# Optimization experiments

Hardware: AMD Instinct MI355X
Metric: run time of the kernel (lower is better)

Reference implementation:

```python
import jax, jax.numpy as jnp
import numpy as np

B, S, D = 2, 2048, 1024
H = 16
HD = D // H  # head_dim = 64


def setup_inputs() -> dict:
    key = jax.random.key(0)
    ks = jax.random.split(key, 9)
    std = 1.0 / np.sqrt(HD)
    inp = {
        "X": jax.random.normal(ks[0], (B, S, D), dtype=jnp.float32),
        # per-head Q/K/V Linear weights stacked: [H, head_dim, head_dim], biases [H, head_dim]
        "Wq": jax.random.uniform(ks[1], (H, HD, HD), jnp.float32, -std, std),
        "bq": jax.random.uniform(ks[2], (H, HD), jnp.float32, -std, std),
        "Wk": jax.random.uniform(ks[3], (H, HD, HD), jnp.float32, -std, std),
        "bk": jax.random.uniform(ks[4], (H, HD), jnp.float32, -std, std),
        "Wv": jax.random.uniform(ks[5], (H, HD, HD), jnp.float32, -std, std),
        "bv": jax.random.uniform(ks[6], (H, HD), jnp.float32, -std, std),
        # output projection: [D, D] (in, out layout), bias [D]
        "Wo": jax.random.uniform(ks[7], (D, D), jnp.float32, -1.0 / np.sqrt(D), 1.0 / np.sqrt(D)),
        "bo": jax.random.uniform(ks[8], (D,), jnp.float32, -1.0 / np.sqrt(D), 1.0 / np.sqrt(D)),
    }
    return inp


def reference(X, Wq, bq, Wk, bk, Wv, bv, Wo, bo):
    # Split hidden dim into heads: [B, S, H, HD]
    x = X.reshape(B, S, H, HD)
    scale = jnp.sqrt(jnp.asarray(HD, dtype=X.dtype))
    # Per-head linear projections (batched over heads)
    Q = jnp.einsum("bshd,hde->bshe", x, Wq) + bq
    K = jnp.einsum("bshd,hde->bshe", x, Wk) + bk
    V = jnp.einsum("bshd,hde->bshe", x, Wv) + bv
    # Attention scores [B, H, S, S]
    scores = jnp.einsum("bshd,bthd->bhst", Q, K) / scale
    attn = jax.nn.softmax(scores, axis=-1)
    # Weighted values -> [B, S, H, HD] -> concat -> [B, S, D]
    out = jnp.einsum("bhst,bthd->bshd", attn, V).reshape(B, S, D)
    return out @ Wo + bo
```

## Files before the change

kernel.cpp:

```cpp
#include <hip/hip_runtime.h>
#include <stdint.h>

#define B_  2
#define S_  2048
#define D_  1024
#define H_  16
#define HD_ 64
#define TOK (B_*S_)

typedef __bf16 bf16x8 __attribute__((ext_vector_type(8)));
typedef __bf16 bf16x4 __attribute__((ext_vector_type(4)));
typedef float  f32x4  __attribute__((ext_vector_type(4)));

static_assert(sizeof(bf16x8) == 16, "bf16x8 must be 16B");
static_assert(sizeof(bf16x4) == 8,  "bf16x4 must be 8B");

__device__ __forceinline__ float fexp2(float x) { return __builtin_amdgcn_exp2f(x); }

__device__ __forceinline__ f32x4 mfma16(bf16x8 a, bf16x8 b, f32x4 c) {
    return __builtin_amdgcn_mfma_f32_16x16x32_bf16(a, b, c, 0, 0, 0);
}

__global__ __launch_bounds__(256) void k_transpose_wo(
    const float* __restrict__ Wo, unsigned short* __restrict__ WoT)
{
    __shared__ float t[64][65];
    const int i0 = blockIdx.x * 64;
    const int o0 = blockIdx.y * 64;
    const int tid = threadIdx.x;
    #pragma unroll
    for (int p = 0; p < 16; ++p) {
        int idx = tid + p * 256;
        int r = idx >> 6, c = idx & 63;
        t[r][c] = Wo[(size_t)(i0 + r) * D_ + o0 + c];
    }
    __syncthreads();
    #pragma unroll
    for (int p = 0; p < 16; ++p) {
        int idx = tid + p * 256;
        int r = idx >> 6, c = idx & 63;
        reinterpret_cast<__bf16*>(WoT)[(size_t)(o0 + r) * D_ + i0 + c] = (__bf16)t[c][r];
    }
}

__global__ __launch_bounds__(256) void k_transpose_w(
    const float* __restrict__ Wq, const float* __restrict__ Wk,
    const float* __restrict__ Wv, unsigned short* __restrict__ WT)
{
    __shared__ float t[64][65];
    const int h = blockIdx.x, z = blockIdx.y;
    const float* W = (z == 0) ? Wq : (z == 1) ? Wk : Wv;
    const int tid = threadIdx.x;
    #pragma unroll
    for (int p = 0; p < 4; ++p) {
        int idx = tid + p * 256;
        int r = idx >> 4, c4 = (idx & 15) * 4;
        *reinterpret_cast<float4*>(&t[r][c4]) =
            *reinterpret_cast<const float4*>(&W[h * 4096 + r * 64 + c4]);
    }
    __syncthreads();
    const int e = tid >> 2, db = (tid & 3) * 16;
    __bf16* out = reinterpret_cast<__bf16*>(WT) + ((size_t)(z * H_ + h) * 64 + e) * 64 + db;
    #pragma unroll
    for (int jj = 0; jj < 2; ++jj) {
        bf16x8 v;
        #pragma unroll
        for (int j = 0; j < 8; ++j) v[j] = (__bf16)t[db + jj * 8 + j][e];
        *reinterpret_cast<bf16x8*>(out + jj * 8) = v;
    }
}

__global__ __launch_bounds__(256) void k_qkv(
    const float* __restrict__ X, const unsigned short* __restrict__ WT,
    const float* __restrict__ bq, const float* __restrict__ bk,
    const float* __restrict__ bv,
    unsigned short* __restrict__ Qo, unsigned short* __restrict__ Ko,
    unsigned short* __restrict__ Vt)
{
    __shared__ unsigned short Xl[128 * 64];
    __shared__ unsigned short Wl[3][64 * 64];

    const int tid  = threadIdx.x;
    const int lane = tid & 63, w = tid >> 6;
    const int g = lane >> 4, q = lane & 15;
    const int tok0 = blockIdx.x * 128;
    const int h    = blockIdx.y;

    #pragma unroll
    for (int i = 0; i < 4; ++i) {
        int c = tid + 256 * i;
        int row = c >> 3, slot = c & 7;
        const float* src = &X[(size_t)(tok0 + row) * D_ + h * HD_ + slot * 8];
        float4 x0 = *reinterpret_cast<const float4*>(src);
        float4 x1 = *reinterpret_cast<const float4*>(src + 4);
        bf16x8 v = { (__bf16)x0.x, (__bf16)x0.y, (__bf16)x0.z, (__bf16)x0.w,
                     (__bf16)x1.x, (__bf16)x1.y, (__bf16)x1.z, (__bf16)x1.w };
        *reinterpret_cast<bf16x8*>(
            reinterpret_cast<char*>(Xl) + row * 128 + ((slot ^ (row & 7)) * 16)) = v;
    }
    #pragma unroll
    for (int zz = 0; zz < 3; ++zz) {
        #pragma unroll
        for (int i = 0; i < 2; ++i) {
            int c = tid + 256 * i;
            int e = c >> 3, slot = c & 7;
            bf16x8 v = *reinterpret_cast<const bf16x8*>(
                &WT[((size_t)(zz * H_ + h) * 64 + e) * 64 + slot * 8]);
            *reinterpret_cast<bf16x8*>(
                reinterpret_cast<char*>(Wl[zz]) + e * 128 + ((slot ^ (e & 7)) * 16)) = v;
        }
    }
    __syncthreads();

    const float scq = 0.18033688011112042f;
    const int b  = tok0 >> 11;
    const int sb = (tok0 & (S_ - 1)) + w * 32;

    #pragma unroll
    for (int z = 0; z < 3; ++z) {
        const float* bb = (z == 0) ? bq : (z == 1) ? bk : bv;
        f32x4 acc[2][4] = {};
        #pragma unroll
        for (int s = 0; s < 2; ++s) {
            bf16x8 af[2], bfr[4];
            #pragma unroll
            for (int am = 0; am < 2; ++am) {
                int row  = w * 32 + am * 16 + q;
                int slot = (s * 4 + g) ^ (row & 7);
                af[am] = *reinterpret_cast<const bf16x8*>(
                    reinterpret_cast<const char*>(Xl) + row * 128 + slot * 16);
            }
            #pragma unroll
            for (int bn = 0; bn < 4; ++bn) {
                int row  = bn * 16 + q;
                int slot = (s * 4 + g) ^ (row & 7);
                bfr[bn] = *reinterpret_cast<const bf16x8*>(
                    reinterpret_cast<const char*>(Wl[z]) + row * 128 + slot * 16);
            }
            if (z == 2) {
                #pragma unroll
                for (int am = 0; am < 2; ++am)
                    #pragma unroll
                    for (int bn = 0; bn < 4; ++bn)
                        acc[am][bn] = mfma16(af[am], bfr[bn], acc[am][bn]);
            } else {
                #pragma unroll
                for (int am = 0; am < 2; ++am)
                    #pragma unroll
                    for (int bn = 0; bn < 4; ++bn)
                        acc[am][bn] = mfma16(bfr[bn], af[am], acc[am][bn]);
            }
        }
        if (z == 2) {
            #pragma unroll
            for (int bn = 0; bn < 4; ++bn) {
                int e = bn * 16 + q;
                float bia = bb[h * HD_ + e];
                #pragma unroll
                for (int am = 0; am < 2; ++am) {
                    int s4 = sb + am * 16 + 4 * g;
                    bf16x4 ov = { (__bf16)(acc[am][bn][0] + bia), (__bf16)(acc[am][bn][1] + bia),
                                  (__bf16)(acc[am][bn][2] + bia), (__bf16)(acc[am][bn][3] + bia) };
                    *reinterpret_cast<bf16x4*>(
                        &Vt[((size_t)(b * H_ + h) * HD_ + e) * S_ + s4]) = ov;
                }
            }
        } else {
            const float sc = (z == 0) ? scq : 1.0f;
            unsigned short* dst = (z == 0) ? Qo : Ko;
            #pragma unroll
            for (int bn = 0; bn < 4; ++bn) {
                float4 bia4 = *reinterpret_cast<const float4*>(&bb[h * HD_ + bn * 16 + 4 * g]);
                #pragma unroll
                for (int am = 0; am < 2; ++am) {
                    int tok = sb + am * 16 + q;
                    bf16x4 ov = { (__bf16)((acc[am][bn][0] + bia4.x) * sc),
                                  (__bf16)((acc[am][bn][1] + bia4.y) * sc),
                                  (__bf16)((acc[am][bn][2] + bia4.z) * sc),
                                  (__bf16)((acc[am][bn][3] + bia4.w) * sc) };
                    *reinterpret_cast<bf16x4*>(
                        &dst[((size_t)(b * H_ + h) * S_ + tok) * HD_ + bn * 16 + 4 * g]) = ov;
                }
            }
        }
    }
}

__global__ __launch_bounds__(256) void k_attn(
    const unsigned short* __restrict__ Q,
    const unsigned short* __restrict__ K,
    const unsigned short* __restrict__ V,
    unsigned short* __restrict__ O)
{
    __shared__ unsigned short K_lds[2][32 * 72];
    __shared__ unsigned short V_lds[2][64 * 40];
    __shared__ unsigned short P_lds[4][32 * 40];

    const int bh = blockIdx.y;
    const unsigned short* Qp = Q + (size_t)bh * S_ * HD_;
    const unsigned short* Kp = K + (size_t)bh * S_ * HD_;
    const unsigned short* Vp = V + (size_t)bh * HD_ * S_;

    const int tid  = threadIdx.x;
    const int lane = tid & 63, w = tid >> 6;
    const int g = lane >> 4, q = lane & 15;
    const int q0   = blockIdx.x * 128 + w * 32;
    const int rowA = q0 + q, rowB = q0 + 16 + q;

    bf16x8 qfA0 = *reinterpret_cast<const bf16x8*>(&Qp[(size_t)rowA * HD_ + 8 * g]);
    bf16x8 qfA1 = *reinterpret_cast<const bf16x8*>(&Qp[(size_t)rowA * HD_ + 32 + 8 * g]);
    bf16x8 qfB0 = *reinterpret_cast<const bf16x8*>(&Qp[(size_t)rowB * HD_ + 8 * g]);
    bf16x8 qfB1 = *reinterpret_cast<const bf16x8*>(&Qp[(size_t)rowB * HD_ + 32 + 8 * g]);

    f32x4 accA[4] = {}, accB[4] = {};
    float mA = -3.0e38f, mB = -3.0e38f, lA = 0.0f, lB = 0.0f;

    const int kr = tid >> 3, ks = (tid & 7) * 8;
    const int vr = tid >> 2, vs = (tid & 3) * 8;
    unsigned short* Pw = P_lds[w];

    const unsigned short* kSrc = Kp + (size_t)kr * HD_ + ks;
    const unsigned short* vSrc = Vp + (size_t)vr * S_  + vs;

    {
        uint4 k0 = *reinterpret_cast<const uint4*>(kSrc);
        uint4 v0 = *reinterpret_cast<const uint4*>(vSrc);
        *reinterpret_cast<uint4*>(&K_lds[0][kr * 72 + ks]) = k0;
        *reinterpret_cast<uint4*>(&V_lds[0][vr * 40 + vs]) = v0;
    }
    __syncthreads();

    const int NT = S_ / 32;
    for (int t = 0; t < NT; ++t) {
        const int cur = t & 1, nxt = cur ^ 1;

        uint4 kn, vn;
        const bool more = (t + 1 < NT);
        if (more) {
            kn = *reinterpret_cast<const uint4*>(kSrc + (size_t)(t + 1) * 32 * HD_);
            vn = *reinterpret_cast<const uint4*>(vSrc + (size_t)(t + 1) * 32);
        }

        const unsigned short* Kb = K_lds[cur];
        const unsigned short* Vb = V_lds[cur];
        bf16x8 k00 = *reinterpret_cast<const bf16x8*>(&Kb[q * 72 + 8 * g]);
        bf16x8 k01 = *reinterpret_cast<const bf16x8*>(&Kb[q * 72 + 32 + 8 * g]);
        bf16x8 k10 = *reinterpret_cast<const bf16x8*>(&Kb[(16 + q) * 72 + 8 * g]);
        bf16x8 k11 = *reinterpret_cast<const bf16x8*>(&Kb[(16 + q) * 72 + 32 + 8 * g]);
        bf16x8 vf0 = *reinterpret_cast<const bf16x8*>(&Vb[(0 * 16 + q) * 40 + 8 * g]);
        bf16x8 vf1 = *reinterpret_cast<const bf16x8*>(&Vb[(1 * 16 + q) * 40 + 8 * g]);
        bf16x8 vf2 = *reinterpret_cast<const bf16x8*>(&Vb[(2 * 16 + q) * 40 + 8 * g]);
        bf16x8 vf3 = *reinterpret_cast<const bf16x8*>(&Vb[(3 * 16 + q) * 40 + 8 * g]);

        f32x4 z4 = {0.f, 0.f, 0.f, 0.f};
        f32x4 sA0 = mfma16(k00, qfA0, z4); sA0 = mfma16(k01, qfA1, sA0);
        f32x4 sA1 = mfma16(k10, qfA0, z4); sA1 = mfma16(k11, qfA1, sA1);
        f32x4 sB0 = mfma16(k00, qfB0, z4); sB0 = mfma16(k01, qfB1, sB0);
        f32x4 sB1 = mfma16(k10, qfB0, z4); sB1 = mfma16(k11, qfB1, sB1);

        float pmA = fmaxf(fmaxf(fmaxf(sA0[0], sA0[1]), fmaxf(sA0[2], sA0[3])),
                          fmaxf(fmaxf(sA1[0], sA1[1]), fmaxf(sA1[2], sA1[3])));
        float pmB = fmaxf(fmaxf(fmaxf(sB0[0], sB0[1]), fmaxf(sB0[2], sB0[3])),
                          fmaxf(fmaxf(sB1[0], sB1[1]), fmaxf(sB1[2], sB1[3])));
        if (!__all((pmA - mA <= 8.0f) && (pmB - mB <= 8.0f))) {
            float rA = pmA;
            rA = fmaxf(rA, __shfl_xor(rA, 16));
            rA = fmaxf(rA, __shfl_xor(rA, 32));
            float mnA = fmaxf(mA, rA);
            float sclA = fexp2(mA - mnA);
            mA = mnA; lA *= sclA;
            accA[0] *= sclA; accA[1] *= sclA; accA[2] *= sclA; accA[3] *= sclA;
            float rB = pmB;
            rB = fmaxf(rB, __shfl_xor(rB, 16));
            rB = fmaxf(rB, __shfl_xor(rB, 32));
            float mnB = fmaxf(mB, rB);
            float sclB = fexp2(mB - mnB);
            mB = mnB; lB *= sclB;
            accB[0] *= sclB; accB[1] *= sclB; accB[2] *= sclB; accB[3] *= sclB;
        }
        float pA0 = fexp2(sA0[0] - mA), pA1 = fexp2(sA0[1] - mA);
        float pA2 = fexp2(sA0[2] - mA), pA3 = fexp2(sA0[3] - mA);
        float pA4 = fexp2(sA1[0] - mA), pA5 = fexp2(sA1[1] - mA);
        float pA6 = fexp2(sA1[2] - mA), pA7 = fexp2(sA1[3] - mA);
        float pB0 = fexp2(sB0[0] - mB), pB1 = fexp2(sB0[1] - mB);
        float pB2 = fexp2(sB0[2] - mB), pB3 = fexp2(sB0[3] - mB);
        float pB4 = fexp2(sB1[0] - mB), pB5 = fexp2(sB1[1] - mB);
        float pB6 = fexp2(sB1[2] - mB), pB7 = fexp2(sB1[3] - mB);
        lA += ((pA0 + pA1) + (pA2 + pA3)) + ((pA4 + pA5) + (pA6 + pA7));
        lB += ((pB0 + pB1) + (pB2 + pB3)) + ((pB4 + pB5) + (pB6 + pB7));

        bf16x4 a0 = { (__bf16)pA0, (__bf16)pA1, (__bf16)pA2, (__bf16)pA3 };
        bf16x4 a1 = { (__bf16)pA4, (__bf16)pA5, (__bf16)pA6, (__bf16)pA7 };
        bf16x4 b0 = { (__bf16)pB0, (__bf16)pB1, (__bf16)pB2, (__bf16)pB3 };
        bf16x4 b1 = { (__bf16)pB4, (__bf16)pB5, (__bf16)pB6, (__bf16)pB7 };
        *reinterpret_cast<bf16x4*>(&Pw[q * 40 + 4 * g])             = a0;
        *reinterpret_cast<bf16x4*>(&Pw[q * 40 + 16 + 4 * g])        = a1;
        *reinterpret_cast<bf16x4*>(&Pw[(16 + q) * 40 + 4 * g])      = b0;
        *reinterpret_cast<bf16x4*>(&Pw[(16 + q) * 40 + 16 + 4 * g]) = b1;

        bf16x8 pfA = *reinterpret_cast<const bf16x8*>(&Pw[q * 40 + 8 * g]);
        bf16x8 pfB = *reinterpret_cast<const bf16x8*>(&Pw[(16 + q) * 40 + 8 * g]);
        accA[0] = mfma16(vf0, pfA, accA[0]);
        accA[1] = mfma16(vf1, pfA, accA[1]);
        accA[2] = mfma16(vf2, pfA, accA[2]);
        accA[3] = mfma16(vf3, pfA, accA[3]);
        accB[0] = mfma16(vf0, pfB, accB[0]);
        accB[1] = mfma16(vf1, pfB, accB[1]);
        accB[2] = mfma16(vf2, pfB, accB[2]);
        accB[3] = mfma16(vf3, pfB, accB[3]);

        if (more) {
            *reinterpret_cast<uint4*>(&K_lds[nxt][kr * 72 + ks]) = kn;
            *reinterpret_cast<uint4*>(&V_lds[nxt][vr * 40 + vs]) = vn;
        }
        __syncthreads();
    }

    lA += __shfl_xor(lA, 16);  lA += __shfl_xor(lA, 32);
    lB += __shfl_xor(lB, 16);  lB += __shfl_xor(lB, 32);
    const float invA = 1.0f / lA, invB = 1.0f / lB;
    const int b = bh >> 4, h = bh & 15;
    __bf16* Ob = reinterpret_cast<__bf16*>(O);
    size_t rA_ = (size_t)(b * S_ + rowA) * D_ + h * HD_ + 4 * g;
    size_t rB_ = (size_t)(b * S_ + rowB) * D_ + h * HD_ + 4 * g;
    #pragma unroll
    for (int d = 0; d < 4; ++d) {
        bf16x4 oa = { (__bf16)(accA[d][0]*invA), (__bf16)(accA[d][1]*invA),
                      (__bf16)(accA[d][2]*invA), (__bf16)(accA[d][3]*invA) };
        bf16x4 ob = { (__bf16)(accB[d][0]*invB), (__bf16)(accB[d][1]*invB),
                      (__bf16)(accB[d][2]*invB), (__bf16)(accB[d][3]*invB) };
        *reinterpret_cast<bf16x4*>(&Ob[rA_ + 16 * d]) = oa;
        *reinterpret_cast<bf16x4*>(&Ob[rB_ + 16 * d]) = ob;
    }
}

__global__ __launch_bounds__(256) void k_out(
    const unsigned short* __restrict__ A,
    const unsigned short* __restrict__ Wt,
    const float* __restrict__ bo,
    float* __restrict__ C)
{
    __shared__ unsigned short Al[2][128 * 64];
    __shared__ unsigned short Bl[2][128 * 64];

    const int tid  = threadIdx.x;
    const int lane = tid & 63, w = tid >> 6;
    const int g = lane >> 4, q = lane & 15;
    const int wr = w & 1, wc = w >> 1;
    const int m0 = blockIdx.x * 128;
    const int n0 = blockIdx.y * 128;

    int    sbyte[4];
    size_t sgA[4], sgB[4];
    #pragma unroll
    for (int i = 0; i < 4; ++i) {
        int c = tid + 256 * i;
        int row = c >> 3, slot = c & 7;
        sbyte[i] = row * 128 + ((slot ^ (row & 7)) * 16);
        sgA[i] = (size_t)(m0 + row) * D_ + slot * 8;
        sgB[i] = (size_t)(n0 + row) * D_ + slot * 8;
    }

    uint4 ra[4], rb[4];
    #pragma unroll
    for (int i = 0; i < 4; ++i) {
        ra[i] = *reinterpret_cast<const uint4*>(A  + sgA[i]);
        rb[i] = *reinterpret_cast<const uint4*>(Wt + sgB[i]);
    }
    #pragma unroll
    for (int i = 0; i < 4; ++i) {
        *reinterpret_cast<uint4*>(reinterpret_cast<char*>(Al[0]) + sbyte[i]) = ra[i];
        *reinterpret_cast<uint4*>(reinterpret_cast<char*>(Bl[0]) + sbyte[i]) = rb[i];
    }
    __syncthreads();

    f32x4 acc[4][4] = {};
    const int NKT = D_ / 64;
    for (int kt = 0; kt < NKT; ++kt) {
        const int cur = kt & 1, nxt = cur ^ 1;
        const bool more = (kt + 1 < NKT);
        if (more) {
            #pragma unroll
            for (int i = 0; i < 4; ++i) {
                ra[i] = *reinterpret_cast<const uint4*>(A  + sgA[i] + (kt + 1) * 64);
                rb[i] = *reinterpret_cast<const uint4*>(Wt + sgB[i] + (kt + 1) * 64);
            }
        }
        const char* Ab = reinterpret_cast<const char*>(Al[cur]);
        const char* Bb = reinterpret_cast<const char*>(Bl[cur]);
        #pragma unroll
        for (int s = 0; s < 2; ++s) {
            bf16x8 af[4], bfr[4];
            #pragma unroll
            for (int am = 0; am < 4; ++am) {
                int row  = wr * 64 + am * 16 + q;
                int slot = (s * 4 + g) ^ (row & 7);
                af[am] = *reinterpret_cast<const bf16x8*>(Ab + row * 128 + slot * 16);
            }
            #pragma unroll
            for (int bn = 0; bn < 4; ++bn) {
                int row  = wc * 64 + bn * 16 + q;
                int slot = (s * 4 + g) ^ (row & 7);
                bfr[bn] = *reinterpret_cast<const bf16x8*>(Bb + row * 128 + slot * 16);
            }
            #pragma unroll
            for (int am = 0; am < 4; ++am)
                #pragma unroll
                for (int bn = 0; bn < 4; ++bn)
                    acc[am][bn] = mfma16(af[am], bfr[bn], acc[am][bn]);
        }
        if (more) {
            #pragma unroll
            for (int i = 0; i < 4; ++i) {
                *reinterpret_cast<uint4*>(reinterpret_cast<char*>(Al[nxt]) + sbyte[i]) = ra[i];
                *reinterpret_cast<uint4*>(reinterpret_cast<char*>(Bl[nxt]) + sbyte[i]) = rb[i];
            }
        }
        __syncthreads();
    }

    #pragma unroll
    for (int bn = 0; bn < 4; ++bn) {
        int n = n0 + wc * 64 + bn * 16 + q;
        float bia = bo[n];
        #pragma unroll
        for (int am = 0; am < 4; ++am) {
            int mbase = m0 + wr * 64 + am * 16 + 4 * g;
            #pragma unroll
            for (int j = 0; j < 4; ++j)
                C[(size_t)(mbase + j) * D_ + n] = acc[am][bn][j] + bia;
        }
    }
}

extern "C" void kernel_launch(void* const* d_in, const int* in_sizes, int n_in,
                              void* d_out, int out_size, void* d_ws, size_t ws_size,
                              hipStream_t stream)
{
    const float* X  = (const float*)d_in[0];
    const float* Wq = (const float*)d_in[1];
    const float* bq = (const float*)d_in[2];
    const float* Wk = (const float*)d_in[3];
    const float* bk = (const float*)d_in[4];
    const float* Wv = (const float*)d_in[5];
    const float* bv = (const float*)d_in[6];
    const float* Wo = (const float*)d_in[7];
    const float* bo = (const float*)d_in[8];
    float* out = (float*)d_out;

    unsigned short* ws = (unsigned short*)d_ws;
    const size_t QN = (size_t)B_ * H_ * S_ * HD_;
    unsigned short* Qb    = ws;
    unsigned short* Kb    = ws + QN;
    unsigned short* Vtb   = ws + 2 * QN;
    unsigned short* Ob    = ws + 3 * QN;
    unsigned short* WoT   = ws + 4 * QN;
    unsigned short* WqkvT = ws + 4 * QN + (size_t)D_ * D_;

    k_transpose_wo<<<dim3(16, 16), 256, 0, stream>>>(Wo, WoT);
    k_transpose_w<<<dim3(H_, 3), 256, 0, stream>>>(Wq, Wk, Wv, WqkvT);
    k_qkv<<<dim3(TOK / 128, H_), 256, 0, stream>>>(X, WqkvT, bq, bk, bv, Qb, Kb, Vtb);
    k_attn<<<dim3(S_ / 128, B_ * H_), 256, 0, stream>>>(Qb, Kb, Vtb, Ob);
    k_out<<<dim3(TOK / 128, D_ / 128), 256, 0, stream>>>(Ob, WoT, bo, out);
}
```

Baseline: 186.7 us.

## Stage QKV stores through LDS, drop P LDS roundtrip, remap attn blocks, shrink out tiles

The QKV kernel now stages each projection tile in a swizzled LDS buffer so global stores of Q, K and transposed V become full 16-byte coalesced writes. The attention kernel permutes K rows in LDS so the softmax probabilities can be fed to the PV MFMA straight from registers instead of through a per-wave LDS buffer. It also remaps block indices across heads for better spread across the device and raises wave priority around the MFMA bursts. The output GEMM tile shrinks from 128x128 to 64x64 to launch more blocks, at the cost of less reuse per block and extra barriers in the QKV kernel.

New measurement: 172.3 us. -7.7%, faster.

```diff
diff --git a/kernel.cpp b/kernel.cpp
--- a/kernel.cpp
+++ b/kernel.cpp
@@ -79,6 +79,7 @@
 {
     __shared__ unsigned short Xl[128 * 64];
     __shared__ unsigned short Wl[3][64 * 64];
+    __shared__ unsigned short Ml[128 * 64];
 
     const int tid  = threadIdx.x;
     const int lane = tid & 63, w = tid >> 6;
@@ -113,8 +114,9 @@
     __syncthreads();
 
     const float scq = 0.18033688011112042f;
-    const int b  = tok0 >> 11;
-    const int sb = (tok0 & (S_ - 1)) + w * 32;
+    const int b       = tok0 >> 11;
+    const int tokbase = tok0 & (S_ - 1);
+    const int sbw     = w * 32;
 
     #pragma unroll
     for (int z = 0; z < 3; ++z) {
@@ -125,7 +127,7 @@
             bf16x8 af[2], bfr[4];
             #pragma unroll
             for (int am = 0; am < 2; ++am) {
-                int row  = w * 32 + am * 16 + q;
+                int row  = sbw + am * 16 + q;
                 int slot = (s * 4 + g) ^ (row & 7);
                 af[am] = *reinterpret_cast<const bf16x8*>(
                     reinterpret_cast<const char*>(Xl) + row * 128 + slot * 16);
@@ -151,6 +153,7 @@
                         acc[am][bn] = mfma16(bfr[bn], af[am], acc[am][bn]);
             }
         }
+
         if (z == 2) {
             #pragma unroll
             for (int bn = 0; bn < 4; ++bn) {
@@ -158,30 +161,56 @@
                 float bia = bb[h * HD_ + e];
                 #pragma unroll
                 for (int am = 0; am < 2; ++am) {
-                    int s4 = sb + am * 16 + 4 * g;
+                    int tokl  = sbw + am * 16 + 4 * g;
+                    int chunk = tokl >> 3;
                     bf16x4 ov = { (__bf16)(acc[am][bn][0] + bia), (__bf16)(acc[am][bn][1] + bia),
                                   (__bf16)(acc[am][bn][2] + bia), (__bf16)(acc[am][bn][3] + bia) };
                     *reinterpret_cast<bf16x4*>(
-                        &Vt[((size_t)(b * H_ + h) * HD_ + e) * S_ + s4]) = ov;
+                        reinterpret_cast<char*>(Ml) + e * 256 +
+                        ((chunk ^ (e & 15)) * 16) + (g & 1) * 8) = ov;
                 }
             }
+            __syncthreads();
+            #pragma unroll
+            for (int p4 = 0; p4 < 4; ++p4) {
+                int e = p4 * 16 + (tid >> 4);
+                int chunk = tid & 15;
+                bf16x8 v = *reinterpret_cast<const bf16x8*>(
+                    reinterpret_cast<const char*>(Ml) + e * 256 + ((chunk ^ (e & 15)) * 16));
+                *reinterpret_cast<bf16x8*>(
+                    &Vt[((size_t)(b * H_ + h) * HD_ + e) * S_ + tokbase + chunk * 8]) = v;
+            }
+            __syncthreads();
         } else {
             const float sc = (z == 0) ? scq : 1.0f;
-            unsigned short* dst = (z == 0) ? Qo : Ko;
             #pragma unroll
             for (int bn = 0; bn < 4; ++bn) {
                 float4 bia4 = *reinterpret_cast<const float4*>(&bb[h * HD_ + bn * 16 + 4 * g]);
+                int slot = 2 * bn + (g >> 1);
                 #pragma unroll
                 for (int am = 0; am < 2; ++am) {
-                    int tok = sb + am * 16 + q;
+                    int tokl = sbw + am * 16 + q;
                     bf16x4 ov = { (__bf16)((acc[am][bn][0] + bia4.x) * sc),
                                   (__bf16)((acc[am][bn][1] + bia4.y) * sc),
                                   (__bf16)((acc[am][bn][2] + bia4.z) * sc),
                                   (__bf16)((acc[am][bn][3] + bia4.w) * sc) };
                     *reinterpret_cast<bf16x4*>(
-                        &dst[((size_t)(b * H_ + h) * S_ + tok) * HD_ + bn * 16 + 4 * g]) = ov;
+                        reinterpret_cast<char*>(Ml) + tokl * 128 +
+                        ((slot ^ (tokl & 7)) * 16) + (g & 1) * 8) = ov;
                 }
             }
+            __syncthreads();
+            unsigned short* dst = (z == 0) ? Qo : Ko;
+            #pragma unroll
+            for (int p4 = 0; p4 < 4; ++p4) {
+                int row = p4 * 32 + (tid >> 3);
+                int chunk = tid & 7;
+                bf16x8 v = *reinterpret_cast<const bf16x8*>(
+                    reinterpret_cast<const char*>(Ml) + row * 128 + ((chunk ^ (row & 7)) * 16));
+                *reinterpret_cast<bf16x8*>(
+                    &dst[((size_t)(b * H_ + h) * S_ + tokbase + row) * HD_ + chunk * 8]) = v;
+            }
+            __syncthreads();
         }
     }
 }
@@ -194,9 +223,11 @@
 {
     __shared__ unsigned short K_lds[2][32 * 72];
     __shared__ unsigned short V_lds[2][64 * 40];
-    __shared__ unsigned short P_lds[4][32 * 40];
-
-    const int bh = blockIdx.y;
+
+    const int L  = blockIdx.x + (int)gridDim.x * blockIdx.y;
+    const int bh = (L & 7) * 4 + ((L >> 3) & 3);
+    const int sb = L >> 5;
+
     const unsigned short* Qp = Q + (size_t)bh * S_ * HD_;
     const unsigned short* Kp = K + (size_t)bh * S_ * HD_;
     const unsigned short* Vp = V + (size_t)bh * HD_ * S_;
@@ -204,7 +235,7 @@
     const int tid  = threadIdx.x;
     const int lane = tid & 63, w = tid >> 6;
     const int g = lane >> 4, q = lane & 15;
-    const int q0   = blockIdx.x * 128 + w * 32;
+    const int q0   = sb * 128 + w * 32;
     const int rowA = q0 + q, rowB = q0 + 16 + q;
 
     bf16x8 qfA0 = *reinterpret_cast<const bf16x8*>(&Qp[(size_t)rowA * HD_ + 8 * g]);
@@ -217,7 +248,8 @@
 
     const int kr = tid >> 3, ks = (tid & 7) * 8;
     const int vr = tid >> 2, vs = (tid & 3) * 8;
-    unsigned short* Pw = P_lds[w];
+    const int krp = (kr & 4) ? (16 + 4 * (kr >> 3) + (kr & 3))
+                             : (4 * (kr >> 3) + (kr & 3));
 
     const unsigned short* kSrc = Kp + (size_t)kr * HD_ + ks;
     const unsigned short* vSrc = Vp + (size_t)vr * S_  + vs;
@@ -225,8 +257,8 @@
     {
         uint4 k0 = *reinterpret_cast<const uint4*>(kSrc);
         uint4 v0 = *reinterpret_cast<const uint4*>(vSrc);
-        *reinterpret_cast<uint4*>(&K_lds[0][kr * 72 + ks]) = k0;
-        *reinterpret_cast<uint4*>(&V_lds[0][vr * 40 + vs]) = v0;
+        *reinterpret_cast<uint4*>(&K_lds[0][krp * 72 + ks]) = k0;
+        *reinterpret_cast<uint4*>(&V_lds[0][vr * 40 + vs])  = v0;
     }
     __syncthreads();
 
@@ -253,10 +285,12 @@
         bf16x8 vf3 = *reinterpret_cast<const bf16x8*>(&Vb[(3 * 16 + q) * 40 + 8 * g]);
 
         f32x4 z4 = {0.f, 0.f, 0.f, 0.f};
+        __builtin_amdgcn_s_setprio(1);
         f32x4 sA0 = mfma16(k00, qfA0, z4); sA0 = mfma16(k01, qfA1, sA0);
         f32x4 sA1 = mfma16(k10, qfA0, z4); sA1 = mfma16(k11, qfA1, sA1);
         f32x4 sB0 = mfma16(k00, qfB0, z4); sB0 = mfma16(k01, qfB1, sB0);
         f32x4 sB1 = mfma16(k10, qfB0, z4); sB1 = mfma16(k11, qfB1, sB1);
+        __builtin_amdgcn_s_setprio(0);
 
         float pmA = fmaxf(fmaxf(fmaxf(sA0[0], sA0[1]), fmaxf(sA0[2], sA0[3])),
                           fmaxf(fmaxf(sA1[0], sA1[1]), fmaxf(sA1[2], sA1[3])));
@@ -289,17 +323,12 @@
         lA += ((pA0 + pA1) + (pA2 + pA3)) + ((pA4 + pA5) + (pA6 + pA7));
         lB += ((pB0 + pB1) + (pB2 + pB3)) + ((pB4 + pB5) + (pB6 + pB7));
 
-        bf16x4 a0 = { (__bf16)pA0, (__bf16)pA1, (__bf16)pA2, (__bf16)pA3 };
-        bf16x4 a1 = { (__bf16)pA4, (__bf16)pA5, (__bf16)pA6, (__bf16)pA7 };
-        bf16x4 b0 = { (__bf16)pB0, (__bf16)pB1, (__bf16)pB2, (__bf16)pB3 };
-        bf16x4 b1 = { (__bf16)pB4, (__bf16)pB5, (__bf16)pB6, (__bf16)pB7 };
-        *reinterpret_cast<bf16x4*>(&Pw[q * 40 + 4 * g])             = a0;
-        *reinterpret_cast<bf16x4*>(&Pw[q * 40 + 16 + 4 * g])        = a1;
-        *reinterpret_cast<bf16x4*>(&Pw[(16 + q) * 40 + 4 * g])      = b0;
-        *reinterpret_cast<bf16x4*>(&Pw[(16 + q) * 40 + 16 + 4 * g]) = b1;
-
-        bf16x8 pfA = *reinterpret_cast<const bf16x8*>(&Pw[q * 40 + 8 * g]);
-        bf16x8 pfB = *reinterpret_cast<const bf16x8*>(&Pw[(16 + q) * 40 + 8 * g]);
+        bf16x8 pfA = { (__bf16)pA0, (__bf16)pA1, (__bf16)pA2, (__bf16)pA3,
+                       (__bf16)pA4, (__bf16)pA5, (__bf16)pA6, (__bf16)pA7 };
+        bf16x8 pfB = { (__bf16)pB0, (__bf16)pB1, (__bf16)pB2, (__bf16)pB3,
+                       (__bf16)pB4, (__bf16)pB5, (__bf16)pB6, (__bf16)pB7 };
+
+        __builtin_amdgcn_s_setprio(1);
         accA[0] = mfma16(vf0, pfA, accA[0]);
         accA[1] = mfma16(vf1, pfA, accA[1]);
         accA[2] = mfma16(vf2, pfA, accA[2]);
@@ -308,10 +337,11 @@
         accB[1] = mfma16(vf1, pfB, accB[1]);
         accB[2] = mfma16(vf2, pfB, accB[2]);
         accB[3] = mfma16(vf3, pfB, accB[3]);
+        __builtin_amdgcn_s_setprio(0);
 
         if (more) {
-            *reinterpret_cast<uint4*>(&K_lds[nxt][kr * 72 + ks]) = kn;
-            *reinterpret_cast<uint4*>(&V_lds[nxt][vr * 40 + vs]) = vn;
+            *reinterpret_cast<uint4*>(&K_lds[nxt][krp * 72 + ks]) = kn;
+            *reinterpret_cast<uint4*>(&V_lds[nxt][vr * 40 + vs])  = vn;
         }
         __syncthreads();
     }
@@ -340,20 +370,20 @@
     const float* __restrict__ bo,
     float* __restrict__ C)
 {
-    __shared__ unsigned short Al[2][128 * 64];
-    __shared__ unsigned short Bl[2][128 * 64];
+    __shared__ unsigned short Al[2][64 * 64];
+    __shared__ unsigned short Bl[2][64 * 64];
 
     const int tid  = threadIdx.x;
     const int lane = tid & 63, w = tid >> 6;
     const int g = lane >> 4, q = lane & 15;
     const int wr = w & 1, wc = w >> 1;
-    const int m0 = blockIdx.x * 128;
-    const int n0 = blockIdx.y * 128;
-
-    int    sbyte[4];
-    size_t sgA[4], sgB[4];
-    #pragma unroll
-    for (int i = 0; i < 4; ++i) {
+    const int m0 = blockIdx.x * 64;
+    const int n0 = blockIdx.y * 64;
+
+    int    sbyte[2];
+    size_t sgA[2], sgB[2];
+    #pragma unroll
+    for (int i = 0; i < 2; ++i) {
         int c = tid + 256 * i;
         int row = c >> 3, slot = c & 7;
         sbyte[i] = row * 128 + ((slot ^ (row & 7)) * 16);
@@ -361,27 +391,27 @@
         sgB[i] = (size_t)(n0 + row) * D_ + slot * 8;
     }
 
-    uint4 ra[4], rb[4];
-    #pragma unroll
-    for (int i = 0; i < 4; ++i) {
+    uint4 ra[2], rb[2];
+    #pragma unroll
+    for (int i = 0; i < 2; ++i) {
         ra[i] = *reinterpret_cast<const uint4*>(A  + sgA[i]);
         rb[i] = *reinterpret_cast<const uint4*>(Wt + sgB[i]);
     }
     #pragma unroll
-    for (int i = 0; i < 4; ++i) {
+    for (int i = 0; i < 2; ++i) {
         *reinterpret_cast<uint4*>(reinterpret_cast<char*>(Al[0]) + sbyte[i]) = ra[i];
         *reinterpret_cast<uint4*>(reinterpret_cast<char*>(Bl[0]) + sbyte[i]) = rb[i];
     }
     __syncthreads();
 
-    f32x4 acc[4][4] = {};
+    f32x4 acc[2][2] = {};
     const int NKT = D_ / 64;
     for (int kt = 0; kt < NKT; ++kt) {
         const int cur = kt & 1, nxt = cur ^ 1;
         const bool more = (kt + 1 < NKT);
         if (more) {
             #pragma unroll
-            for (int i = 0; i < 4; ++i) {
+            for (int i = 0; i < 2; ++i) {
                 ra[i] = *reinterpret_cast<const uint4*>(A  + sgA[i] + (kt + 1) * 64);
                 rb[i] = *reinterpret_cast<const uint4*>(Wt + sgB[i] + (kt + 1) * 64);
             }
@@ -390,28 +420,28 @@
         const char* Bb = reinterpret_cast<const char*>(Bl[cur]);
         #pragma unroll
         for (int s = 0; s < 2; ++s) {
-            bf16x8 af[4], bfr[4];
-            #pragma unroll
-            for (int am = 0; am < 4; ++am) {
-                int row  = wr * 64 + am * 16 + q;
+            bf16x8 af[2], bfr[2];
+            #pragma unroll
+            for (int am = 0; am < 2; ++am) {
+                int row  = wr * 32 + am * 16 + q;
                 int slot = (s * 4 + g) ^ (row & 7);
                 af[am] = *reinterpret_cast<const bf16x8*>(Ab + row * 128 + slot * 16);
             }
             #pragma unroll
-            for (int bn = 0; bn < 4; ++bn) {
-                int row  = wc * 64 + bn * 16 + q;
+            for (int bn = 0; bn < 2; ++bn) {
+                int row  = wc * 32 + bn * 16 + q;
                 int slot = (s * 4 + g) ^ (row & 7);
                 bfr[bn] = *reinterpret_cast<const bf16x8*>(Bb + row * 128 + slot * 16);
             }
             #pragma unroll
-            for (int am = 0; am < 4; ++am)
+            for (int am = 0; am < 2; ++am)
                 #pragma unroll
-                for (int bn = 0; bn < 4; ++bn)
+                for (int bn = 0; bn < 2; ++bn)
                     acc[am][bn] = mfma16(af[am], bfr[bn], acc[am][bn]);
         }
         if (more) {
             #pragma unroll
-            for (int i = 0; i < 4; ++i) {
+            for (int i = 0; i < 2; ++i) {
                 *reinterpret_cast<uint4*>(reinterpret_cast<char*>(Al[nxt]) + sbyte[i]) = ra[i];
                 *reinterpret_cast<uint4*>(reinterpret_cast<char*>(Bl[nxt]) + sbyte[i]) = rb[i];
             }
@@ -420,12 +450,12 @@
     }
 
     #pragma unroll
-    for (int bn = 0; bn < 4; ++bn) {
-        int n = n0 + wc * 64 + bn * 16 + q;
+    for (int bn = 0; bn < 2; ++bn) {
+        int n = n0 + wc * 32 + bn * 16 + q;
         float bia = bo[n];
         #pragma unroll
-        for (int am = 0; am < 4; ++am) {
-            int mbase = m0 + wr * 64 + am * 16 + 4 * g;
+        for (int am = 0; am < 2; ++am) {
+            int mbase = m0 + wr * 32 + am * 16 + 4 * g;
             #pragma unroll
             for (int j = 0; j < 4; ++j)
                 C[(size_t)(mbase + j) * D_ + n] = acc[am][bn][j] + bia;
@@ -460,6 +490,6 @@
     k_transpose_wo<<<dim3(16, 16), 256, 0, stream>>>(Wo, WoT);
     k_transpose_w<<<dim3(H_, 3), 256, 0, stream>>>(Wq, Wk, Wv, WqkvT);
     k_qkv<<<dim3(TOK / 128, H_), 256, 0, stream>>>(X, WqkvT, bq, bk, bv, Qb, Kb, Vtb);
-    k_attn<<<dim3(S_ / 128, B_ * H_), 256, 0, stream>>>(Qb, Kb, Vtb, Ob);
-    k_out<<<dim3(TOK / 128, D_ / 128), 256, 0, stream>>>(Ob, WoT, bo, out);
-}
+    k_attn<<<dim3(16, 32), 256, 0, stream>>>(Qb, Kb, Vtb, Ob);
+    k_out<<<dim3(TOK / 64, D_ / 64), 256, 0, stream>>>(Ob, WoT, bo, out);
+}
```
